# Kernel tuning notes

Hardware: AMD Instinct MI355X
Metric: run time of the kernel (lower is better)

The kernel has to match this reference:

```python
import jax, jax.numpy as jnp
import numpy as np

B, S, D, H, L = 32, 512, 1024, 1024, 2


def _lstm_layer(inp, h, c, w_ih, w_hh, b):
    # inp: [B,S,Din]; precompute input projection once (as in the torch code)
    x_proj = jnp.einsum('bsd,dg->bsg', inp, w_ih) + b  # [B,S,4H]
    Hdim = h.shape[-1]

    def step(carry, xt):
        h, c = carry
        gates = xt + h @ w_hh  # [B,4H]
        i = jax.nn.sigmoid(gates[:, :Hdim])
        f = jax.nn.sigmoid(gates[:, Hdim:2 * Hdim])
        g = jnp.tanh(gates[:, 2 * Hdim:3 * Hdim])
        o = jax.nn.sigmoid(gates[:, 3 * Hdim:])
        c = f * c + i * g
        h = o * jnp.tanh(c)
        return (h, c), h

    (h, c), ys = jax.lax.scan(step, (h, c), jnp.swapaxes(x_proj, 0, 1))
    return jnp.swapaxes(ys, 0, 1), h, c  # [B,S,H]


def setup_inputs() -> dict:
    key = jax.random.key(0)
    ks = jax.random.split(key, 7)
    r = 0.1
    def u(k, shape):
        return jax.random.uniform(k, shape, jnp.float32, -r, r)
    b0 = jnp.zeros((4 * H,), jnp.float32).at[H:2 * H].set(1.0)
    b1 = jnp.zeros((4 * H,), jnp.float32).at[H:2 * H].set(1.0)
    return {
        'x': jax.random.normal(ks[0], (B, S, D), jnp.float32),
        'h0': jnp.zeros((L, B, H), jnp.float32),
        'c0': jnp.zeros((L, B, H), jnp.float32),
        'w_ih0': u(ks[1], (D, 4 * H)),
        'w_hh0': u(ks[2], (H, 4 * H)),
        'b0': b0,
        'w_ih1': u(ks[3], (H, 4 * H)),
        'w_hh1': u(ks[4], (H, 4 * H)),
        'b1': b1,
    }


def reference(x, h0, c0, w_ih0, w_hh0, b0, w_ih1, w_hh1, b1):
    # Dropouts are 0 (eval-mode LockedDropout is identity).
    y0, h_0, c_0 = _lstm_layer(x, h0[0], c0[0], w_ih0, w_hh0, b0)
    y1, h_1, c_1 = _lstm_layer(y0, h0[1], c0[1], w_ih1, w_hh1, b1)
    h_n = jnp.stack([h_0, h_1], axis=0)
    c_n = jnp.stack([c_0, c_1], axis=0)
    return y1, h_n, c_n
```

## Files before the change

### kernel.cpp

```cpp
#include <hip/hip_runtime.h>
#include <hip/hip_cooperative_groups.h>
#include <cstddef>

#define Bq 32
#define Sq 512
#define Hq 1024
#define G4q 4096
#define CHUNKq 128
#define NCHq (Sq / CHUNKq)
#define BHq (Bq * Hq)

__global__ __launch_bounds__(256)
void gemm_xproj(const float* __restrict__ A,
                const float* __restrict__ Wm,
                const float* __restrict__ bias,
                float* __restrict__ gates,
                unsigned int* __restrict__ bar,
                int s0)
{
    __shared__ float As[8][132];
    __shared__ float Bs[8][132];

    const int tid = threadIdx.x;
    if (blockIdx.x == 0 && blockIdx.y == 0 && tid < 18)
        bar[tid * 32] = 0u;

    const int tr = tid >> 4;
    const int tc = tid & 15;
    const int m0 = blockIdx.y * 128;
    const int n0 = blockIdx.x * 128;

    float acc[8][8];
    #pragma unroll
    for (int i = 0; i < 8; ++i)
        #pragma unroll
        for (int j = 0; j < 8; ++j) acc[i][j] = 0.f;

    const int a_m  = tid >> 1;
    const int a_k4 = (tid & 1) * 4;
    const int b_k  = tid >> 5;
    const int b_n4 = (tid & 31) * 4;

    const int am_g = m0 + a_m;
    const int ab = am_g >> 7;
    const int as = s0 + (am_g & 127);
    const float* Arow = A + ((size_t)ab * Sq + as) * 1024;

    for (int k0 = 0; k0 < 1024; k0 += 8) {
        float4 av = *(const float4*)(Arow + k0 + a_k4);
        float4 bv = *(const float4*)(Wm + (size_t)(k0 + b_k) * G4q + n0 + b_n4);
        __syncthreads();
        As[a_k4 + 0][a_m] = av.x;
        As[a_k4 + 1][a_m] = av.y;
        As[a_k4 + 2][a_m] = av.z;
        As[a_k4 + 3][a_m] = av.w;
        *(float4*)(&Bs[b_k][b_n4]) = bv;
        __syncthreads();
        #pragma unroll
        for (int kk = 0; kk < 8; ++kk) {
            float4 a0 = *(const float4*)(&As[kk][tr * 8]);
            float4 a1 = *(const float4*)(&As[kk][tr * 8 + 4]);
            float4 b0 = *(const float4*)(&Bs[kk][tc * 8]);
            float4 b1 = *(const float4*)(&Bs[kk][tc * 8 + 4]);
            float avv[8] = {a0.x, a0.y, a0.z, a0.w, a1.x, a1.y, a1.z, a1.w};
            float bvv[8] = {b0.x, b0.y, b0.z, b0.w, b1.x, b1.y, b1.z, b1.w};
            #pragma unroll
            for (int i = 0; i < 8; ++i)
                #pragma unroll
                for (int j = 0; j < 8; ++j)
                    acc[i][j] += avv[i] * bvv[j];
        }
    }

    float bv8[8];
    *(float4*)(bv8)     = *(const float4*)(bias + n0 + tc * 8);
    *(float4*)(bv8 + 4) = *(const float4*)(bias + n0 + tc * 8 + 4);

    #pragma unroll
    for (int i = 0; i < 8; ++i) {
        const int m = m0 + tr * 8 + i;
        const int b = m >> 7;
        const int r = m & 127;
        float* outp = gates + ((size_t)r * Bq + b) * G4q + n0 + tc * 8;
        float4 v0 = {acc[i][0] + bv8[0], acc[i][1] + bv8[1],
                     acc[i][2] + bv8[2], acc[i][3] + bv8[3]};
        float4 v1 = {acc[i][4] + bv8[4], acc[i][5] + bv8[5],
                     acc[i][6] + bv8[6], acc[i][7] + bv8[7]};
        *(float4*)outp       = v0;
        *(float4*)(outp + 4) = v1;
    }
}

__global__ __launch_bounds__(512, 2)
void lstm_scan(const float* __restrict__ gates,
               const float* __restrict__ Whh,
               float* __restrict__ hbuf,
               float* __restrict__ cstate,
               float* __restrict__ y,
               unsigned int* __restrict__ bar,
               int t0)
{
    __shared__ float4 Wlds[4096];

    const int tid  = threadIdx.x;
    const int lane = tid & 63;
    const int bg   = tid >> 6;
    const int j0   = blockIdx.x * 4;
    const int kg   = lane;

    #pragma unroll
    for (int idx = tid; idx < 4096; idx += 512) {
        const int k  = idx >> 2;
        const int s  = idx & 3;
        const int kgs = k >> 4;
        const int slot = (s + (kgs >> 1)) & 3;
        Wlds[(((k & 15) * 64 + kgs) << 2) + slot] =
            *(const float4*)(Whh + (size_t)k * G4q + s * Hq + j0);
    }

    const int bi = ((lane & 1) << 1) | ((lane >> 1) & 1);
    const int ct = (((lane >> 2) & 1) << 1) | ((lane >> 3) & 1);
    const int jj = (((lane >> 4) & 1) << 1) | ((lane >> 5) & 1);
    const int b  = bg * 4 + bi;
    const int j  = j0 + jj;

    float creg = cstate[b * Hq + j];
    const float* gbase = gates + (size_t)b * G4q + j;

    __syncthreads();

    for (int tt = 0; tt < CHUNKq; ++tt) {
        const float* ht = hbuf + (tt & 1) * BHq;
        float* hw = hbuf + ((tt + 1) & 1) * BHq;

        const float* gp = gbase + (size_t)tt * Bq * G4q;
        const float g0 = gp[0];
        const float g1 = gp[Hq];
        const float g2 = gp[2 * Hq];
        const float g3 = gp[3 * Hq];

        float4 hv[16];
        const float* hp = ht + kg * 16 * Bq + bg * 4;
        #pragma unroll
        for (int i = 0; i < 16; ++i) {
            asm volatile("global_load_dwordx4 %0, %1, off offset:%c2 sc0 sc1"
                         : "=v"(hv[i]) : "v"(hp), "n"(i * 128));
        }
        asm volatile("s_waitcnt vmcnt(0)" ::: "memory");
        __builtin_amdgcn_sched_barrier(0);

        float work[64];
        #pragma unroll
        for (int v = 0; v < 64; ++v) work[v] = 0.f;

        const float4* wrow = Wlds + (kg << 2);
        #pragma unroll
        for (int i = 0; i < 16; ++i) {
            const float4 h4 = hv[i];
            const float4* wr = wrow + i * 256;
            #pragma unroll
            for (int s = 0; s < 4; ++s) {
                const int slot = (s + (kg >> 1)) & 3;
                const float4 w4 = wr[slot];
                #pragma unroll
                for (int bb = 0; bb < 4; ++bb) {
                    const float hb = (bb == 0) ? h4.x : (bb == 1) ? h4.y
                                   : (bb == 2) ? h4.z : h4.w;
                    work[bb * 16 + s * 4 + 0] += hb * w4.x;
                    work[bb * 16 + s * 4 + 1] += hb * w4.y;
                    work[bb * 16 + s * 4 + 2] += hb * w4.z;
                    work[bb * 16 + s * 4 + 3] += hb * w4.w;
                }
            }
        }

        #define RR(m, n)                                                     \
        {                                                                    \
            const bool hi = (lane & (m)) != 0;                               \
            _Pragma("unroll")                                                \
            for (int i = 0; i < (n); ++i) {                                  \
                const float send = hi ? work[i] : work[i + (n)];             \
                const float got  = __shfl_xor(send, (m), 64);                \
                const float keep = hi ? work[i + (n)] : work[i];             \
                work[i] = keep + got;                                        \
            }                                                                \
        }
        RR(1, 32) RR(2, 16) RR(4, 8) RR(8, 4) RR(16, 2) RR(32, 1)
        #undef RR

        const float a0 = work[0];
        const float a1 = __shfl_xor(work[0], 8, 64);
        const float a2 = __shfl_xor(work[0], 4, 64);
        const float a3 = __shfl_xor(work[0], 12, 64);
        #define SEL(p) (((ct ^ (p)) == 0) ? a0 : ((ct ^ (p)) == 1) ? a1 \
                      : ((ct ^ (p)) == 2) ? a2 : a3)
        const float gi = g0 + SEL(0);
        const float gf = g1 + SEL(1);
        const float gg = g2 + SEL(2);
        const float go = g3 + SEL(3);
        #undef SEL

        const float iv = 1.f / (1.f + expf(-gi));
        const float fv = 1.f / (1.f + expf(-gf));
        const float gv = tanhf(gg);
        const float ov = 1.f / (1.f + expf(-go));
        creg = fv * creg + iv * gv;
        const float hval = ov * tanhf(creg);

        if ((lane & 12) == 0) {
            __hip_atomic_store(hw + j * Bq + b, hval,
                               __ATOMIC_RELAXED, __HIP_MEMORY_SCOPE_AGENT);
            y[((size_t)b * Sq + (t0 + tt)) * Hq + j] = hval;
        }

        __syncthreads();
        if (tid == 0) {
            const int gid = blockIdx.x >> 4;
            unsigned int old = __hip_atomic_fetch_add(bar + gid * 32, 1u,
                                  __ATOMIC_RELAXED, __HIP_MEMORY_SCOPE_AGENT);
            if ((old & 15u) == 15u) {
                unsigned int r = __hip_atomic_fetch_add(bar + 16 * 32, 1u,
                                  __ATOMIC_RELAXED, __HIP_MEMORY_SCOPE_AGENT);
                if ((r & 15u) == 15u)
                    __hip_atomic_store(bar + 17 * 32, (unsigned int)(tt + 1),
                                  __ATOMIC_RELAXED, __HIP_MEMORY_SCOPE_AGENT);
            }
            unsigned int guard = 0;
            while (__hip_atomic_load(bar + 17 * 32, __ATOMIC_RELAXED,
                                     __HIP_MEMORY_SCOPE_AGENT)
                       < (unsigned int)(tt + 1)
                   && ++guard < (1u << 20))
                __builtin_amdgcn_s_sleep(1);
        }
        __syncthreads();
    }

    if ((lane & 12) == 0) cstate[b * Hq + j] = creg;
}

__global__ __launch_bounds__(256)
void h_to_t(const float* __restrict__ src, float* __restrict__ dst) {
    const int i = blockIdx.x * 256 + threadIdx.x;
    const int b = i >> 10, j = i & 1023;
    dst[j * Bq + b] = src[i];
}
__global__ __launch_bounds__(256)
void h_from_t(const float* __restrict__ src, float* __restrict__ dst) {
    const int i = blockIdx.x * 256 + threadIdx.x;
    const int b = i >> 10, j = i & 1023;
    dst[i] = src[j * Bq + b];
}

extern "C" void kernel_launch(void* const* d_in, const int* in_sizes, int n_in,
                              void* d_out, int out_size, void* d_ws, size_t ws_size,
                              hipStream_t stream)
{
    const float* x    = (const float*)d_in[0];
    const float* h0   = (const float*)d_in[1];
    const float* c0   = (const float*)d_in[2];
    const float* wih0 = (const float*)d_in[3];
    const float* whh0 = (const float*)d_in[4];
    const float* b0   = (const float*)d_in[5];
    const float* wih1 = (const float*)d_in[6];
    const float* whh1 = (const float*)d_in[7];
    const float* b1   = (const float*)d_in[8];

    float* out = (float*)d_out;
    float* y1  = out;
    float* hn  = out + (size_t)Bq * Sq * Hq;
    float* cn  = hn + 2 * BHq;

    float* ws    = (float*)d_ws;
    float* gates = ws;
    float* hbuf  = gates + (size_t)CHUNKq * Bq * G4q;
    float* cst   = hbuf + 2 * BHq;
    unsigned int* bar = (unsigned int*)(cst + BHq);

    float* y0 = y1;

    for (int l = 0; l < 2; ++l) {
        const float* Ain  = l ? y0   : x;
        const float* wih  = l ? wih1 : wih0;
        const float* whh  = l ? whh1 : whh0;
        const float* bias = l ? b1   : b0;
        float* yout       = l ? y1   : y0;

        h_to_t<<<128, 256, 0, stream>>>(h0 + (size_t)l * BHq, hbuf);
        hipMemcpyAsync(cst, c0 + (size_t)l * BHq, BHq * sizeof(float),
                       hipMemcpyDeviceToDevice, stream);

        for (int ch = 0; ch < NCHq; ++ch) {
            const int s0 = ch * CHUNKq;
            gemm_xproj<<<dim3(32, 32), 256, 0, stream>>>(Ain, wih, bias,
                                                         gates, bar, s0);

            const float* garg = gates;
            const float* warg = whh;
            float* harg = hbuf;
            float* carg = cst;
            float* yarg = yout;
            unsigned int* barg = bar;
            int targ = s0;
            void* kp[] = {(void*)&garg, (void*)&warg, (void*)&harg,
                          (void*)&carg, (void*)&yarg, (void*)&barg,
                          (void*)&targ};
            hipLaunchCooperativeKernel((void*)lstm_scan, dim3(256), dim3(512),
                                       kp, 0, stream);
        }

        h_from_t<<<128, 256, 0, stream>>>(hbuf, hn + (size_t)l * BHq);
        hipMemcpyAsync(cn + (size_t)l * BHq, cst, BHq * sizeof(float),
                       hipMemcpyDeviceToDevice, stream);
    }
}
```

Baseline: 17.95 ms.

## Reorder gate precompute layout and prefetch next-step gates in LSTM scan

The input-projection GEMM now writes gates in a blocked layout grouped by hidden-column quad, gate, and batch, so each scan block's gate values for a timestep sit contiguously. The scan kernel loads the next timestep's gates during the current step, keeping that global load off the serial recurrence critical path. Only the lanes that update state load gates and compute activations, which removes the redundant select logic. The change touches both kernels and their shared buffer indexing, so a layout mismatch would silently corrupt results.

```diff
diff --git a/kernel.cpp b/kernel.cpp
--- a/kernel.cpp
+++ b/kernel.cpp
@@ -76,18 +76,23 @@
     *(float4*)(bv8)     = *(const float4*)(bias + n0 + tc * 8);
     *(float4*)(bv8 + 4) = *(const float4*)(bias + n0 + tc * 8 + 4);
 
+    const int p  = n0 >> 10;
+    const int nn = (n0 & 1023) + tc * 8;
+    const int j4 = nn >> 2;
+
     #pragma unroll
     for (int i = 0; i < 8; ++i) {
         const int m = m0 + tr * 8 + i;
         const int b = m >> 7;
         const int r = m & 127;
-        float* outp = gates + ((size_t)r * Bq + b) * G4q + n0 + tc * 8;
+        float* outp = gates +
+            ((((size_t)r * 256 + j4) * 4 + p) * 32 + b) * 4;
         float4 v0 = {acc[i][0] + bv8[0], acc[i][1] + bv8[1],
                      acc[i][2] + bv8[2], acc[i][3] + bv8[3]};
         float4 v1 = {acc[i][4] + bv8[4], acc[i][5] + bv8[5],
                      acc[i][6] + bv8[6], acc[i][7] + bv8[7]};
-        *(float4*)outp       = v0;
-        *(float4*)(outp + 4) = v1;
+        *(float4*)outp         = v0;
+        *(float4*)(outp + 512) = v1;
     }
 }
 
@@ -105,7 +110,8 @@
     const int tid  = threadIdx.x;
     const int lane = tid & 63;
     const int bg   = tid >> 6;
-    const int j0   = blockIdx.x * 4;
+    const int bk   = blockIdx.x;
+    const int j0   = bk * 4;
     const int kg   = lane;
 
     #pragma unroll
@@ -123,9 +129,20 @@
     const int jj = (((lane >> 4) & 1) << 1) | ((lane >> 5) & 1);
     const int b  = bg * 4 + bi;
     const int j  = j0 + jj;
+    const bool upd = (lane & 12) == 0;
 
     float creg = cstate[b * Hq + j];
-    const float* gbase = gates + (size_t)b * G4q + j;
+
+    const float* gbase = gates + ((size_t)bk * 4) * 128 + b * 4 + jj;
+    #define GSTEP ((size_t)256 * 4 * 128)
+
+    float gpre0 = 0.f, gpre1 = 0.f, gpre2 = 0.f, gpre3 = 0.f;
+    if (upd) {
+        gpre0 = gbase[0];
+        gpre1 = gbase[128];
+        gpre2 = gbase[256];
+        gpre3 = gbase[384];
+    }
 
     __syncthreads();
 
@@ -133,12 +150,6 @@
         const float* ht = hbuf + (tt & 1) * BHq;
         float* hw = hbuf + ((tt + 1) & 1) * BHq;
 
-        const float* gp = gbase + (size_t)tt * Bq * G4q;
-        const float g0 = gp[0];
-        const float g1 = gp[Hq];
-        const float g2 = gp[2 * Hq];
-        const float g3 = gp[3 * Hq];
-
         float4 hv[16];
         const float* hp = ht + kg * 16 * Bq + bg * 4;
         #pragma unroll
@@ -148,6 +159,16 @@
         }
         asm volatile("s_waitcnt vmcnt(0)" ::: "memory");
         __builtin_amdgcn_sched_barrier(0);
+
+        const float g0 = gpre0, g1 = gpre1, g2 = gpre2, g3 = gpre3;
+        const int tn = (tt < CHUNKq - 1) ? tt + 1 : tt;
+        if (upd) {
+            const float* gp = gbase + (size_t)tn * GSTEP;
+            gpre0 = gp[0];
+            gpre1 = gp[128];
+            gpre2 = gp[256];
+            gpre3 = gp[384];
+        }
 
         float work[64];
         #pragma unroll
@@ -192,22 +213,18 @@
         const float a1 = __shfl_xor(work[0], 8, 64);
         const float a2 = __shfl_xor(work[0], 4, 64);
         const float a3 = __shfl_xor(work[0], 12, 64);
-        #define SEL(p) (((ct ^ (p)) == 0) ? a0 : ((ct ^ (p)) == 1) ? a1 \
-                      : ((ct ^ (p)) == 2) ? a2 : a3)
-        const float gi = g0 + SEL(0);
-        const float gf = g1 + SEL(1);
-        const float gg = g2 + SEL(2);
-        const float go = g3 + SEL(3);
-        #undef SEL
-
-        const float iv = 1.f / (1.f + expf(-gi));
-        const float fv = 1.f / (1.f + expf(-gf));
-        const float gv = tanhf(gg);
-        const float ov = 1.f / (1.f + expf(-go));
-        creg = fv * creg + iv * gv;
-        const float hval = ov * tanhf(creg);
-
-        if ((lane & 12) == 0) {
+
+        if (upd) {
+            const float gi = g0 + a0;
+            const float gf = g1 + a1;
+            const float gg = g2 + a2;
+            const float go = g3 + a3;
+            const float iv = 1.f / (1.f + expf(-gi));
+            const float fv = 1.f / (1.f + expf(-gf));
+            const float gv = tanhf(gg);
+            const float ov = 1.f / (1.f + expf(-go));
+            creg = fv * creg + iv * gv;
+            const float hval = ov * tanhf(creg);
             __hip_atomic_store(hw + j * Bq + b, hval,
                                __ATOMIC_RELAXED, __HIP_MEMORY_SCOPE_AGENT);
             y[((size_t)b * Sq + (t0 + tt)) * Hq + j] = hval;
@@ -215,7 +232,7 @@
 
         __syncthreads();
         if (tid == 0) {
-            const int gid = blockIdx.x >> 4;
+            const int gid = bk >> 4;
             unsigned int old = __hip_atomic_fetch_add(bar + gid * 32, 1u,
                                   __ATOMIC_RELAXED, __HIP_MEMORY_SCOPE_AGENT);
             if ((old & 15u) == 15u) {
@@ -235,7 +252,8 @@
         __syncthreads();
     }
 
-    if ((lane & 12) == 0) cstate[b * Hq + j] = creg;
+    if (upd) cstate[b * Hq + j] = creg;
+    #undef GSTEP
 }
 
 __global__ __launch_bounds__(256)
```

After: 18.18 ms. No clear change (+1.3%).
